# Kernel optimization log

Hardware: AMD Instinct MI355X
Metric: run time of the kernel (lower is better)

The kernel has to match this reference:

```python
import jax, jax.numpy as jnp
import numpy as np

N, E, G, B, L = 24576, 98304, 512, 512, 1000
F_IN, H1, C1, C2, HID = 5, 2, 64, 128, 256


def setup_inputs() -> dict:
    key = jax.random.key(0)
    ks = jax.random.split(key, 20)
    rn = lambda k, s: jax.random.normal(k, s, jnp.float32) * 0.1
    return {
        "x": jax.random.normal(ks[0], (N, F_IN), jnp.float32),
        "edge_index": jax.random.randint(ks[1], (2, E), 0, N),
        "batch": jnp.sort(jax.random.randint(ks[2], (N,), 0, G)),
        "protein_seq": jax.random.randint(ks[3], (B, L), 0, 22),
        "W1": rn(ks[4], (F_IN, H1 * C1)), "att_src1": rn(ks[5], (H1, C1)), "att_dst1": rn(ks[6], (H1, C1)), "b1": jnp.zeros((H1 * C1,), jnp.float32),
        "W2": rn(ks[7], (H1 * C1, C2)), "att_src2": rn(ks[8], (1, C2)), "att_dst2": rn(ks[9], (1, C2)), "b2": jnp.zeros((C2,), jnp.float32),
        "Wd": rn(ks[10], (C2, HID)), "bd": jnp.zeros((HID,), jnp.float32),
        "Pe": rn(ks[11], (22, 64)),
        "K1": rn(ks[12], (64, 64, 3)), "bk1": jnp.zeros((64,), jnp.float32),
        "K2": rn(ks[13], (128, 64, 5)), "bk2": jnp.zeros((128,), jnp.float32),
        "Wp": rn(ks[14], (128, HID)), "bp": jnp.zeros((HID,), jnp.float32),
        "Wf1": rn(ks[15], (2 * HID, 128)), "bf1": jnp.zeros((128,), jnp.float32),
        "Wf2": rn(ks[16], (128, 64)), "bf2": jnp.zeros((64,), jnp.float32),
        "Wo": rn(ks[17], (64, 1)), "bo": jnp.zeros((1,), jnp.float32),
    }


def _gat(x, edge_index, W, att_src, att_dst, b, heads, out_ch):
    """PyG GATConv: add self-loops, per-edge LeakyReLU(0.2) scores, segment softmax over dst."""
    n = x.shape[0]
    h = (x @ W).reshape(n, heads, out_ch)
    loop = jnp.arange(n)
    src = jnp.concatenate([edge_index[0], loop])
    dst = jnp.concatenate([edge_index[1], loop])
    a_s = jnp.sum(h * att_src[None], axis=-1)  # [n, H]
    a_d = jnp.sum(h * att_dst[None], axis=-1)
    e = jax.nn.leaky_relu(a_s[src] + a_d[dst], negative_slope=0.2)  # [E+n, H]
    m = jax.ops.segment_max(e, dst, num_segments=n)
    w = jnp.exp(e - m[dst])
    den = jax.ops.segment_sum(w, dst, num_segments=n)
    alpha = w / (den[dst] + 1e-16)
    out = jax.ops.segment_sum(h[src] * alpha[..., None], dst, num_segments=n)
    return out.reshape(n, heads * out_ch) + b


def _conv1d(x, k, pad):  # x: [B,C,L], k: [O,I,K]
    return jax.lax.conv_general_dilated(x, k, (1,), [(pad, pad)], dimension_numbers=("NCH", "OIH", "NCH"))


def reference(x, edge_index, batch, protein_seq, W1, att_src1, att_dst1, b1, W2, att_src2, att_dst2, b2, Wd, bd, Pe, K1, bk1, K2, bk2, Wp, bp, Wf1, bf1, Wf2, bf2, Wo, bo):
    # drug branch (GAT x2 + global mean pool)
    g = jax.nn.elu(_gat(x, edge_index, W1, att_src1, att_dst1, b1, H1, C1))
    g = jax.nn.elu(_gat(g, edge_index, W2, att_src2, att_dst2, b2, 1, C2))
    sums = jax.ops.segment_sum(g, batch, num_segments=G)
    cnt = jax.ops.segment_sum(jnp.ones((g.shape[0], 1), g.dtype), batch, num_segments=G)
    drug = jax.nn.relu(sums / jnp.maximum(cnt, 1.0) @ Wd + bd)
    # protein branch (embed -> conv1d x2 -> global max pool)
    pe = Pe[protein_seq].transpose(0, 2, 1)  # [B, 64, L]
    p = jax.nn.elu(_conv1d(pe, K1, 1) + bk1[None, :, None])
    p = jax.nn.elu(_conv1d(p, K2, 2) + bk2[None, :, None])
    prot = jax.nn.relu(jnp.max(p, axis=2) @ Wp + bp)
    # head
    h = jnp.concatenate([drug, prot], axis=1)
    h = jax.nn.relu(h @ Wf1 + bf1)
    h = jax.nn.relu(h @ Wf2 + bf2)
    return h @ Wo + bo
```

## Files before the change

### kernel.cpp

```cpp
#include <hip/hip_runtime.h>
#include <hip/hip_bf16.h>
#include <math.h>

#define NN 24576
#define NE 98304
#define ETOT (NE + NN)
#define NG 512
#define NB 512
#define LL 1000
#define TL 124
#define NTILE 9
#define PROT_BLKS (NB * NTILE)
#define CNT_BLKS (ETOT / 256)
#define AS1_BLKS (NN * 2 / 256)

typedef __attribute__((ext_vector_type(8))) short short8;
typedef __attribute__((ext_vector_type(4))) short short4v;
typedef __attribute__((ext_vector_type(4))) float f32x4;

__device__ inline short f2bf(float x) {
    union { __hip_bfloat16 b; short s; } u;
    u.b = __float2bfloat16(x);
    return u.s;
}

__device__ inline float bf2f(short s) {
    return __uint_as_float(((unsigned)(unsigned short)s) << 16);
}

__device__ inline void atomicMaxFloat(float* addr, float val) {
    int* ai = (int*)addr;
    int old = __float_as_int(*addr);
    while (__int_as_float(old) < val) {
        int assumed = old;
        old = atomicCAS(ai, assumed, __float_as_int(val));
        if (old == assumed) break;
    }
}

__global__ void k_init_prep(int* deg, int* cursor, float* sums, float* cnt, float* pmax,
                            const float* K1, const float* K2, const float* W2, const float* Pe,
                            const float* W1, const float* as1c, const float* ad1c,
                            const float* as2c, const float* ad2c,
                            short* Bswz1, short* Bswz2, short* Bh2, short* Bl2, short* Peb,
                            float* wvec) {
    int bid = blockIdx.x, t = threadIdx.x;
    if (bid < 256) {
        int i = bid * 256 + t;
        if (i < NN) { deg[i] = 0; cursor[i] = 0; }
        if (i < NG * 128) sums[i] = 0.f;
        if (i < NG) cnt[i] = 0.f;
        if (i < NB * 128) pmax[i] = -1e30f;
        return;
    }
    int idx = (bid - 256) * 256 + t;
    if (idx < 22 * 64) Peb[idx] = f2bf(Pe[idx]);
    if (idx < 20) {
        int q = idx % 10, hd = q / 5, f = q % 5;
        const float* av = (idx < 10) ? as1c : ad1c;
        float s = 0.f;
        for (int c = 0; c < 64; c++) s += W1[f * 128 + hd * 64 + c] * av[hd * 64 + c];
        wvec[idx < 10 ? q : 10 + q] = s;
    }
    if (idx >= 32 && idx < 288) {
        int q = idx - 32;
        int kk = q & 127;
        const float* av = (q < 128) ? as2c : ad2c;
        float s = 0.f;
        for (int n2 = 0; n2 < 128; n2++) s += W2[kk * 128 + n2] * av[n2];
        wvec[idx] = s;
    }
    if (idx < 192 * 64) {
        int j = idx & 7, lane = (idx >> 3) & 63, rest = idx >> 9;
        int nt = rest & 3, kb = rest >> 2;
        int k = kb * 32 + ((lane >> 4) << 3) + j;
        int n = nt * 16 + (lane & 15);
        int kk = k >> 6, i = k & 63;
        Bswz1[idx] = f2bf(K1[n * 192 + i * 3 + kk]);
    }
    if (idx < 320 * 128) {
        int j = idx & 7, lane = (idx >> 3) & 63, rest = idx >> 9;
        int nt = rest & 7, kb = rest >> 3;
        int k = kb * 32 + ((lane >> 4) << 3) + j;
        int n = nt * 16 + (lane & 15);
        int kk = k / 64, i = k % 64;
        Bswz2[idx] = f2bf(K2[n * 320 + i * 5 + kk]);
    }
    if (idx < 128 * 128) {
        int j = idx & 7, lane = (idx >> 3) & 63, rest = idx >> 9;
        int nt = rest & 7, kb = rest >> 3;
        int k = kb * 32 + ((lane >> 4) << 3) + j;
        int n = nt * 16 + (lane & 15);
        float v = W2[k * 128 + n];
        short hh = f2bf(v);
        Bh2[idx] = hh;
        Bl2[idx] = f2bf(v - bf2f(hh));
    }
}

#define SSTR 72
__global__ __launch_bounds__(256, 4) void k_prot_cnt_as1(
    const int* seq, const short* Peb, const short* Bswz1, const float* bk1,
    const short* Bswz2, const float* bk2, float* pmax,
    const int* ei, int* deg,
    const float* x, const float* wvec, float* as1o, float* ad1o) {
    int bid = blockIdx.x;
    int t = threadIdx.x;

    if (bid >= PROT_BLKS) {
        int rb = bid - PROT_BLKS;
        if (rb < CNT_BLKS) {
            int e = rb * 256 + t;
            int d = (e < NE) ? ei[NE + e] : e - NE;
            atomicAdd(&deg[d], 1);
        } else {
            int idx = (rb - CNT_BLKS) * 256 + t;
            int n = idx >> 1, hd = idx & 1;
            float s = 0.f, dv = 0.f;
#pragma unroll
            for (int f = 0; f < 5; f++) {
                float xv = x[n * 5 + f];
                s += xv * wvec[hd * 5 + f];
                dv += xv * wvec[10 + hd * 5 + f];
            }
            as1o[idx] = s;
            ad1o[idx] = dv;
        }
        return;
    }

    __shared__ __align__(16) short sEmb[130 * SSTR];
    __shared__ __align__(16) short s1[132 * SSTR];

    int b = bid / NTILE;
    int tile = bid - b * NTILE;
    int t0 = tile * TL;
    int wv = t >> 6, lane = t & 63;
    int ln15 = lane & 15, quad = lane >> 4;
    int mhalf = wv & 1, nhalf = wv >> 1;

    for (int j0 = 0; j0 < 130; j0 += 64) {
        int j = j0 + (t >> 2);
        if (j < 130) {
            int c0 = (t & 3) * 16;
            int l = t0 - 3 + j;
            int id = (l >= 0 && l < LL) ? seq[b * LL + l] : -1;
            short* dst = &sEmb[j * SSTR + c0];
            if (id >= 0) {
                const short8* src = (const short8*)&Peb[id * 64 + c0];
                *(short8*)dst = src[0];
                *(short8*)(dst + 8) = src[1];
            } else {
                *(short8*)dst = (short8){0, 0, 0, 0, 0, 0, 0, 0};
                *(short8*)(dst + 8) = (short8){0, 0, 0, 0, 0, 0, 0, 0};
            }
        }
    }
    s1[(128 + (t >> 6)) * SSTR + (t & 63)] = 0;
    __syncthreads();

    {
        f32x4 acc[4][2];
#pragma unroll
        for (int mi = 0; mi < 4; mi++)
#pragma unroll
            for (int ni = 0; ni < 2; ni++) acc[mi][ni] = (f32x4){0.f, 0.f, 0.f, 0.f};
#pragma unroll
        for (int kb = 0; kb < 6; kb++) {
            int koff = kb * 32 + quad * 8;
            int kk = koff >> 6, i0 = koff & 63;
            short8 b0 = *(const short8*)&Bswz1[((kb * 4 + nhalf * 2 + 0) * 64 + lane) * 8];
            short8 b1 = *(const short8*)&Bswz1[((kb * 4 + nhalf * 2 + 1) * 64 + lane) * 8];
#pragma unroll
            for (int mi = 0; mi < 4; mi++) {
                int arow = (mhalf * 4 + mi) * 16 + ln15 + kk;
                short8 a = *(const short8*)&sEmb[arow * SSTR + i0];
                acc[mi][0] = __builtin_amdgcn_mfma_f32_16x16x32_bf16(a, b0, acc[mi][0], 0, 0, 0);
                acc[mi][1] = __builtin_amdgcn_mfma_f32_16x16x32_bf16(a, b1, acc[mi][1], 0, 0, 0);
            }
        }
#pragma unroll
        for (int mi = 0; mi < 4; mi++) {
            int mt = mhalf * 4 + mi;
#pragma unroll
            for (int ni = 0; ni < 2; ni++) {
                int col = (nhalf * 2 + ni) * 16 + ln15;
                float bias = bk1[col];
#pragma unroll
                for (int r = 0; r < 4; r++) {
                    int q = mt * 16 + quad * 4 + r;
                    int l = t0 - 2 + q;
                    float v = acc[mi][ni][r] + bias;
                    v = v > 0.f ? v : __expf(v) - 1.f;
                    s1[q * SSTR + col] = (l >= 0 && l < LL) ? f2bf(v) : (short)0;
                }
            }
        }
    }
    __syncthreads();

    f32x4 acc2[4][4];
#pragma unroll
    for (int mi = 0; mi < 4; mi++)
#pragma unroll
        for (int ni = 0; ni < 4; ni++) acc2[mi][ni] = (f32x4){0.f, 0.f, 0.f, 0.f};
#pragma unroll 2
    for (int kb = 0; kb < 10; kb++) {
        int koff = kb * 32 + quad * 8;
        int kk = koff >> 6, i0 = koff & 63;
        short8 a[4], bb[4];
#pragma unroll
        for (int mi = 0; mi < 4; mi++) {
            int arow = (mhalf * 4 + mi) * 16 + ln15 + kk;
            a[mi] = *(const short8*)&s1[arow * SSTR + i0];
        }
#pragma unroll
        for (int ni = 0; ni < 4; ni++)
            bb[ni] = *(const short8*)&Bswz2[((kb * 8 + nhalf * 4 + ni) * 64 + lane) * 8];
#pragma unroll
        for (int mi = 0; mi < 4; mi++)
#pragma unroll
            for (int ni = 0; ni < 4; ni++)
                acc2[mi][ni] = __builtin_amdgcn_mfma_f32_16x16x32_bf16(a[mi], bb[ni], acc2[mi][ni], 0, 0, 0);
    }

#pragma unroll
    for (int ni = 0; ni < 4; ni++) {
        int col = (nhalf * 4 + ni) * 16 + ln15;
        float mx = -1e30f;
#pragma unroll
        for (int mi = 0; mi < 4; mi++) {
#pragma unroll
            for (int r = 0; r < 4; r++) {
                int p = (mhalf * 4 + mi) * 16 + quad * 4 + r;
                if (p < TL && t0 + p < LL) mx = fmaxf(mx, acc2[mi][ni][r]);
            }
        }
        mx = fmaxf(mx, __shfl_xor(mx, 16, 64));
        mx = fmaxf(mx, __shfl_xor(mx, 32, 64));
        if (quad == 0) {
            float v = mx + bk2[col];
            v = v > 0.f ? v : __expf(v) - 1.f;
            atomicMaxFloat(&pmax[b * 128 + col], v);
        }
    }
}

__global__ void k_scan1(const int* deg, int* excl, int* part) {
    __shared__ int s[256];
    int b = blockIdx.x, t = threadIdx.x, i = b * 256 + t;
    int v = deg[i];
    s[t] = v;
    __syncthreads();
    for (int o = 1; o < 256; o <<= 1) {
        int x = (t >= o) ? s[t - o] : 0;
        __syncthreads();
        s[t] += x;
        __syncthreads();
    }
    excl[i] = s[t] - v;
    if (t == 255) part[b] = s[t];
}

__global__ void k_scan23(const int* excl, const int* part, int* rowptr) {
    __shared__ int sp[96];
    __shared__ int pref;
    int b = blockIdx.x, t = threadIdx.x;
    if (t < 96) sp[t] = part[t];
    __syncthreads();
    if (t == 0) {
        int run = 0;
        for (int i = 0; i < b; i++) run += sp[i];
        pref = run;
    }
    __syncthreads();
    int i = b * 256 + t;
    rowptr[i] = excl[i] + pref;
    if (i == 0) rowptr[NN] = ETOT;
}

__global__ void k_scatter(const int* ei, const int* rowptr, int* cursor, int* colidx) {
    int e = blockIdx.x * 256 + threadIdx.x;
    if (e >= ETOT) return;
    int s, d;
    if (e < NE) { s = ei[e]; d = ei[NE + e]; }
    else { s = d = e - NE; }
    int pos = atomicAdd(&cursor[d], 1);
    colidx[rowptr[d] + pos] = s;
}

__global__ void k_agg2x(const int* rowptr, const int* colidx, const float* x,
                        const float* as_, const float* ad_,
                        const float* W1, const float* b1, const float* wvec,
                        unsigned int* g1b, float* as2, float* ad2) {
    __shared__ float sW[640];
    __shared__ float sb1[128];
    __shared__ float swa[256];
    int t = threadIdx.x;
    for (int i = t; i < 640; i += 256) sW[i] = W1[i];
    if (t < 128) { sb1[t] = b1[t]; swa[t] = wvec[32 + t]; swa[128 + t] = wvec[160 + t]; }
    __syncthreads();

    int d = blockIdx.x * 16 + (t >> 4);
    int g = t & 15;
    int hd = (g < 5) ? 0 : 1;
    int f = (g < 5) ? g : g - 5;
    float adv = ad_[d * 2 + hd];
    int p0 = rowptr[d], p1 = rowptr[d + 1];
    float den = 0.f, acc = 0.f;
    if (g < 10) {
        for (int pc = p0; pc < p1; pc += 4) {
            int sarr[4]; float ev[4], xv[4];
#pragma unroll
            for (int i = 0; i < 4; i++) {
                int pp = pc + i;
                sarr[i] = colidx[pp < p1 ? pp : p1 - 1];
            }
#pragma unroll
            for (int i = 0; i < 4; i++) {
                ev[i] = as_[sarr[i] * 2 + hd];
                xv[i] = x[sarr[i] * 5 + f];
            }
#pragma unroll
            for (int i = 0; i < 4; i++) {
                if (pc + i < p1) {
                    float e = ev[i] + adv;
                    e = e >= 0.f ? e : 0.2f * e;
                    float w = __expf(e);
                    den += w;
                    acc += w * xv[i];
                }
            }
        }
    }
    float xn = acc / (den + 1e-16f);
    int gb = (t & 63) & ~15;
    int hcol = g >> 3;
    float xs[5];
#pragma unroll
    for (int f2 = 0; f2 < 5; f2++)
        xs[f2] = __shfl(xn, gb + hcol * 5 + f2, 64);
    float ps = 0.f, pd = 0.f;
    float g1v[8];
#pragma unroll
    for (int k = 0; k < 8; k++) {
        int col = g * 8 + k;
        float v = sb1[col];
#pragma unroll
        for (int f2 = 0; f2 < 5; f2++) v += xs[f2] * sW[f2 * 128 + col];
        v = v > 0.f ? v : __expf(v) - 1.f;
        g1v[k] = v;
        ps += v * swa[col];
        pd += v * swa[128 + col];
    }
    uint4 pk;
    pk.x = ((unsigned)(unsigned short)f2bf(g1v[1]) << 16) | (unsigned)(unsigned short)f2bf(g1v[0]);
    pk.y = ((unsigned)(unsigned short)f2bf(g1v[3]) << 16) | (unsigned)(unsigned short)f2bf(g1v[2]);
    pk.z = ((unsigned)(unsigned short)f2bf(g1v[5]) << 16) | (unsigned)(unsigned short)f2bf(g1v[4]);
    pk.w = ((unsigned)(unsigned short)f2bf(g1v[7]) << 16) | (unsigned)(unsigned short)f2bf(g1v[6]);
    *(uint4*)&g1b[d * 64 + g * 4] = pk;
#pragma unroll
    for (int msk = 1; msk < 16; msk <<= 1) {
        ps += __shfl_xor(ps, msk, 64);
        pd += __shfl_xor(pd, msk, 64);
    }
    if (g == 0) { as2[d] = ps; ad2[d] = pd; }
}

__global__ void k_agg1y(const int* rowptr, const int* colidx, const unsigned int* hb,
                        const float* as_, const float* ad_, float* yacc) {
    int t = threadIdx.x;
    int d = blockIdx.x * 4 + (t >> 6);
    int c = t & 63;
    float adv = ad_[d];
    int p0 = rowptr[d], p1 = rowptr[d + 1];
    float den = 0.f, acc0 = 0.f, acc1 = 0.f;
    for (int pc = p0; pc < p1; pc += 4) {
        int sarr[4]; float ev[4]; unsigned int hv[4];
#pragma unroll
        for (int i = 0; i < 4; i++) {
            int pp = pc + i;
            sarr[i] = colidx[pp < p1 ? pp : p1 - 1];
        }
#pragma unroll
        for (int i = 0; i < 4; i++) {
            ev[i] = as_[sarr[i]];
            hv[i] = hb[sarr[i] * 64 + c];
        }
#pragma unroll
        for (int i = 0; i < 4; i++) {
            if (pc + i < p1) {
                float e = ev[i] + adv;
                e = e >= 0.f ? e : 0.2f * e;
                float w = __expf(e);
                den += w;
                acc0 += w * __uint_as_float(hv[i] << 16);
                acc1 += w * __uint_as_float(hv[i] & 0xFFFF0000u);
            }
        }
    }
    float inv = 1.f / (den + 1e-16f);
    ((float2*)yacc)[d * 64 + c] = (float2){acc0 * inv, acc1 * inv};
}

#define ASTR 136
__global__ __launch_bounds__(256, 2) void k_g2mm(
    const float* yacc, const short* Bh, const short* Bl, const float* b2, float* g2) {
    __shared__ __align__(16) short Ah[64 * ASTR];
    __shared__ __align__(16) short Al[64 * ASTR];
    int t = threadIdx.x;
    int m0 = blockIdx.x * 64;
    int wv = t >> 6, lane = t & 63;
    int ln15 = lane & 15, quad = lane >> 4;

    for (int i = t; i < 64 * 32; i += 256) {
        int row = i >> 5, c4 = (i & 31) * 4;
        float4 v = *(const float4*)&yacc[(m0 + row) * 128 + c4];
        short4v hi, lo;
        hi.x = f2bf(v.x); lo.x = f2bf(v.x - bf2f(hi.x));
        hi.y = f2bf(v.y); lo.y = f2bf(v.y - bf2f(hi.y));
        hi.z = f2bf(v.z); lo.z = f2bf(v.z - bf2f(hi.z));
        hi.w = f2bf(v.w); lo.w = f2bf(v.w - bf2f(hi.w));
        *(short4v*)&Ah[row * ASTR + c4] = hi;
        *(short4v*)&Al[row * ASTR + c4] = lo;
    }
    __syncthreads();

    f32x4 acc[8];
#pragma unroll
    for (int nt = 0; nt < 8; nt++) acc[nt] = (f32x4){0.f, 0.f, 0.f, 0.f};
    int arow = wv * 16 + ln15;
#pragma unroll
    for (int kb = 0; kb < 4; kb++) {
        int koff = kb * 32 + quad * 8;
        short8 a_hi = *(const short8*)&Ah[arow * ASTR + koff];
        short8 a_lo = *(const short8*)&Al[arow * ASTR + koff];
#pragma unroll
        for (int nt = 0; nt < 8; nt++) {
            short8 bh = *(const short8*)&Bh[((kb * 8 + nt) * 64 + lane) * 8];
            short8 bl = *(const short8*)&Bl[((kb * 8 + nt) * 64 + lane) * 8];
            acc[nt] = __builtin_amdgcn_mfma_f32_16x16x32_bf16(a_hi, bh, acc[nt], 0, 0, 0);
            acc[nt] = __builtin_amdgcn_mfma_f32_16x16x32_bf16(a_hi, bl, acc[nt], 0, 0, 0);
            acc[nt] = __builtin_amdgcn_mfma_f32_16x16x32_bf16(a_lo, bh, acc[nt], 0, 0, 0);
        }
    }
#pragma unroll
    for (int nt = 0; nt < 8; nt++) {
        int col = nt * 16 + ln15;
        float bias = b2[col];
#pragma unroll
        for (int r = 0; r < 4; r++) {
            float v = acc[nt][r] + bias;
            v = v > 0.f ? v : __expf(v) - 1.f;
            int n = m0 + wv * 16 + quad * 4 + r;
            g2[n * 128 + col] = v;
        }
    }
}

__global__ void k_pool(const float* g2, const int* batch, float* sums, float* cnt) {
    __shared__ int sb[96];
    int blk = blockIdx.x, j = threadIdx.x;
    int n0 = blk * 96;
    if (j < 96) sb[j] = batch[n0 + j];
    __syncthreads();
    float v[4];
#pragma unroll
    for (int i = 0; i < 4; i++) v[i] = g2[(n0 + i) * 128 + j];
    int cur = sb[0], runStart = 0;
    float acc = 0.f;
    for (int q0 = 0; q0 < 96; q0 += 4) {
        float nv[4] = {0.f, 0.f, 0.f, 0.f};
        if (q0 + 4 < 96) {
#pragma unroll
            for (int i = 0; i < 4; i++) nv[i] = g2[(n0 + q0 + 4 + i) * 128 + j];
        }
#pragma unroll
        for (int i = 0; i < 4; i++) {
            int q = q0 + i;
            int bb = sb[q];
            if (bb != cur) {
                atomicAdd(&sums[cur * 128 + j], acc);
                if (j == 0) atomicAdd(&cnt[cur], (float)(q - runStart));
                cur = bb; acc = 0.f; runStart = q;
            }
            acc += v[i];
        }
#pragma unroll
        for (int i = 0; i < 4; i++) v[i] = nv[i];
    }
    atomicAdd(&sums[cur * 128 + j], acc);
    if (j == 0) atomicAdd(&cnt[cur], (float)(96 - runStart));
}

__global__ __launch_bounds__(512) void k_tail(
    const float* pmax, const float* Wp, const float* bp,
    const float* sums, const float* cnt, const float* Wd, const float* bd,
    const float* Wf1, const float* bf1, const float* Wf2, const float* bf2,
    const float* Wo, const float* bo, float* out) {
    __shared__ float in2[512];
    __shared__ float part1[512];
    __shared__ float hh[128];
    __shared__ float part2[512];
    __shared__ float h2s[64];
    int g = blockIdx.x, t = threadIdx.x;

    if (t < 256) {
        float pacc = bp[t];
#pragma unroll 8
        for (int i = 0; i < 128; i++) pacc += pmax[g * 128 + i] * Wp[i * 256 + t];
        in2[256 + t] = pacc > 0.f ? pacc : 0.f;
    } else {
        int o = t - 256;
        float c = cnt[g]; c = c < 1.f ? 1.f : c;
        float inv = 1.f / c;
        float dacc = bd[o];
#pragma unroll 8
        for (int i = 0; i < 128; i++) dacc += sums[g * 128 + i] * inv * Wd[i * 256 + o];
        in2[o] = dacc > 0.f ? dacc : 0.f;
    }
    __syncthreads();

    {
        int o = t >> 2, ks = t & 3;
        float p = 0.f;
        int c0 = ks * 128;
#pragma unroll 8
        for (int cc = c0; cc < c0 + 128; cc++) p += in2[cc] * Wf1[cc * 128 + o];
        part1[t] = p;
    }
    __syncthreads();
    if (t < 128) {
        float a = bf1[t] + part1[t * 4] + part1[t * 4 + 1] + part1[t * 4 + 2] + part1[t * 4 + 3];
        hh[t] = a > 0.f ? a : 0.f;
    }
    __syncthreads();

    {
        int o = t >> 3, ks = t & 7;
        float p = 0.f;
        int c0 = ks * 16;
#pragma unroll
        for (int cc = c0; cc < c0 + 16; cc++) p += hh[cc] * Wf2[cc * 64 + o];
        part2[t] = p;
    }
    __syncthreads();
    if (t < 64) {
        float a = bf2[t];
#pragma unroll
        for (int k = 0; k < 8; k++) a += part2[t * 8 + k];
        h2s[t] = a > 0.f ? a : 0.f;
    }
    __syncthreads();

    if (t < 64) {
        float p = h2s[t] * Wo[t];
#pragma unroll
        for (int off = 32; off > 0; off >>= 1) p += __shfl_down(p, off, 64);
        if (t == 0) out[g] = p + bo[0];
    }
}

extern "C" void kernel_launch(void* const* d_in, const int* in_sizes, int n_in,
                              void* d_out, int out_size, void* d_ws, size_t ws_size,
                              hipStream_t stream) {
    (void)in_sizes; (void)n_in; (void)out_size; (void)ws_size;
    const float* x   = (const float*)d_in[0];
    const int* ei    = (const int*)d_in[1];
    const int* batch = (const int*)d_in[2];
    const int* seq   = (const int*)d_in[3];
    const float* W1  = (const float*)d_in[4];
    const float* a_s1 = (const float*)d_in[5];
    const float* a_d1 = (const float*)d_in[6];
    const float* b1  = (const float*)d_in[7];
    const float* W2  = (const float*)d_in[8];
    const float* a_s2 = (const float*)d_in[9];
    const float* a_d2 = (const float*)d_in[10];
    const float* b2  = (const float*)d_in[11];
    const float* Wd  = (const float*)d_in[12];
    const float* bd  = (const float*)d_in[13];
    const float* Pe  = (const float*)d_in[14];
    const float* K1  = (const float*)d_in[15];
    const float* bk1 = (const float*)d_in[16];
    const float* K2  = (const float*)d_in[17];
    const float* bk2 = (const float*)d_in[18];
    const float* Wp  = (const float*)d_in[19];
    const float* bp  = (const float*)d_in[20];
    const float* Wf1 = (const float*)d_in[21];
    const float* bf1 = (const float*)d_in[22];
    const float* Wf2 = (const float*)d_in[23];
    const float* bf2 = (const float*)d_in[24];
    const float* Wo  = (const float*)d_in[25];
    const float* bo  = (const float*)d_in[26];
    float* out = (float*)d_out;

    float* w = (float*)d_ws;
    float* g1bf = w; w += NN * 64;
    float* yacc = w; w += NN * 128;
    float* g2   = w; w += NN * 128;
    float* as1  = w; w += NN * 2;
    float* ad1  = w; w += NN * 2;
    float* as2  = w; w += NN;
    float* ad2  = w; w += NN;
    float* sums = w; w += NG * 128;
    float* cnt  = w; w += NG;
    float* pmax = w; w += NB * 128;
    float* wvec = w; w += 512;
    short* Bswz1 = (short*)w; w += 192 * 64 / 2;
    short* Bswz2 = (short*)w; w += 320 * 128 / 2;
    short* Bh2  = (short*)w; w += 128 * 128 / 2;
    short* Bl2  = (short*)w; w += 128 * 128 / 2;
    short* Peb  = (short*)w; w += 22 * 64 / 2 + 8;
    int* deg    = (int*)w; w += NN;
    int* cursor = (int*)w; w += NN;
    int* excl   = (int*)w; w += NN;
    int* part   = (int*)w; w += 128;
    int* rowptr = (int*)w; w += NN + 8;
    int* colidx = (int*)w; w += ETOT;

    unsigned int* g1b = (unsigned int*)g1bf;

    hipLaunchKernelGGL(k_init_prep, dim3(256 + 160), dim3(256), 0, stream,
                       deg, cursor, sums, cnt, pmax,
                       K1, K2, W2, Pe, W1, a_s1, a_d1, a_s2, a_d2,
                       Bswz1, Bswz2, Bh2, Bl2, Peb, wvec);

    hipLaunchKernelGGL(k_prot_cnt_as1, dim3(PROT_BLKS + CNT_BLKS + AS1_BLKS), dim3(256), 0, stream,
                       seq, Peb, Bswz1, bk1, Bswz2, bk2, pmax,
                       ei, deg, x, wvec, as1, ad1);

    hipLaunchKernelGGL(k_scan1, dim3(NN / 256), dim3(256), 0, stream, deg, excl, part);
    hipLaunchKernelGGL(k_scan23, dim3(NN / 256), dim3(256), 0, stream, excl, part, rowptr);
    hipLaunchKernelGGL(k_scatter, dim3(ETOT / 256), dim3(256), 0, stream, ei, rowptr, cursor, colidx);

    hipLaunchKernelGGL(k_agg2x, dim3(NN / 16), dim3(256), 0, stream,
                       rowptr, colidx, x, as1, ad1, W1, b1, wvec, g1b, as2, ad2);

    hipLaunchKernelGGL(k_agg1y, dim3(NN / 4), dim3(256), 0, stream,
                       rowptr, colidx, g1b, as2, ad2, yacc);

    hipLaunchKernelGGL(k_g2mm, dim3(NN / 64), dim3(256), 0, stream,
                       yacc, Bh2, Bl2, b2, g2);

    hipLaunchKernelGGL(k_pool, dim3(NN / 96), dim3(128), 0, stream, g2, batch, sums, cnt);

    hipLaunchKernelGGL(k_tail, dim3(NG), dim3(512), 0, stream,
                       pmax, Wp, bp, sums, cnt, Wd, bd, Wf1, bf1, Wf2, bf2, Wo, bo, out);
}
```

Before: 300.6 us.

## Fold embedding into conv1 via per-token lookup table and shrink protein tiles

Since the embedding vocabulary has only 22 tokens, conv1 of the embedded sequence is precomputed as a table M1[token][tap][out_ch] holding K1·Pe. The protein kernel then builds each conv1 output row by summing three table rows plus the bias, which replaces the MFMA conv1 stage and the staging of embeddings in shared memory. Tiles shrink from 124 to 60 positions with all four waves splitting the conv2 output channels, and the occupancy hint rises to 6 blocks. The costs are more blocks with more halo overlap (68 rows computed per 60 outputs) and a fp32 table gather in place of bf16 math, which slightly changes rounding.

After: 294.9 us. No clear change (-1.9%).

```diff
diff --git a/kernel.cpp b/kernel.cpp
--- a/kernel.cpp
+++ b/kernel.cpp
@@ -8,8 +8,8 @@
 #define NG 512
 #define NB 512
 #define LL 1000
-#define TL 124
-#define NTILE 9
+#define TL 60
+#define NTILE 17
 #define PROT_BLKS (NB * NTILE)
 #define CNT_BLKS (ETOT / 256)
 #define AS1_BLKS (NN * 2 / 256)
@@ -42,7 +42,7 @@
                             const float* K1, const float* K2, const float* W2, const float* Pe,
                             const float* W1, const float* as1c, const float* ad1c,
                             const float* as2c, const float* ad2c,
-                            short* Bswz1, short* Bswz2, short* Bh2, short* Bl2, short* Peb,
+                            short* Bswz2, short* Bh2, short* Bl2, float* M1,
                             float* wvec) {
     int bid = blockIdx.x, t = threadIdx.x;
     if (bid < 256) {
@@ -54,7 +54,6 @@
         return;
     }
     int idx = (bid - 256) * 256 + t;
-    if (idx < 22 * 64) Peb[idx] = f2bf(Pe[idx]);
     if (idx < 20) {
         int q = idx % 10, hd = q / 5, f = q % 5;
         const float* av = (idx < 10) ? as1c : ad1c;
@@ -70,13 +69,12 @@
         for (int n2 = 0; n2 < 128; n2++) s += W2[kk * 128 + n2] * av[n2];
         wvec[idx] = s;
     }
-    if (idx < 192 * 64) {
-        int j = idx & 7, lane = (idx >> 3) & 63, rest = idx >> 9;
-        int nt = rest & 3, kb = rest >> 2;
-        int k = kb * 32 + ((lane >> 4) << 3) + j;
-        int n = nt * 16 + (lane & 15);
-        int kk = k >> 6, i = k & 63;
-        Bswz1[idx] = f2bf(K1[n * 192 + i * 3 + kk]);
+    if (idx < 22 * 3 * 64) {
+        int tok = idx / 192, r2 = idx % 192;
+        int k = r2 >> 6, oc = r2 & 63;
+        float s = 0.f;
+        for (int ic = 0; ic < 64; ic++) s += K1[oc * 192 + ic * 3 + k] * Pe[tok * 64 + ic];
+        M1[idx] = s;
     }
     if (idx < 320 * 128) {
         int j = idx & 7, lane = (idx >> 3) & 63, rest = idx >> 9;
@@ -99,8 +97,8 @@
 }
 
 #define SSTR 72
-__global__ __launch_bounds__(256, 4) void k_prot_cnt_as1(
-    const int* seq, const short* Peb, const short* Bswz1, const float* bk1,
+__global__ __launch_bounds__(256, 6) void k_prot_cnt_as1(
+    const int* seq, const float* M1, const float* bk1,
     const short* Bswz2, const float* bk2, float* pmax,
     const int* ei, int* deg,
     const float* x, const float* wvec, float* as1o, float* ad1o) {
@@ -129,110 +127,96 @@
         return;
     }
 
-    __shared__ __align__(16) short sEmb[130 * SSTR];
-    __shared__ __align__(16) short s1[132 * SSTR];
+    __shared__ __align__(16) short s1[68 * SSTR];
+    __shared__ int stok[68];
 
     int b = bid / NTILE;
     int tile = bid - b * NTILE;
     int t0 = tile * TL;
+
+    if (t < 66) {
+        int l = t0 - 3 + t;
+        stok[t] = (l >= 0 && l < LL) ? seq[b * LL + l] : -1;
+    }
+    if (t < 36) {
+        *(short8*)&s1[64 * SSTR + t * 8] = (short8){0, 0, 0, 0, 0, 0, 0, 0};
+    }
+    __syncthreads();
+
+    {
+        int q = t >> 2, c0 = (t & 3) << 4;
+        int l = t0 - 2 + q;
+        short tmp[16];
+        if (l >= 0 && l < LL) {
+            float v[16];
+#pragma unroll
+            for (int j = 0; j < 4; j++) {
+                float4 bv = *(const float4*)&bk1[c0 + j * 4];
+                v[j * 4 + 0] = bv.x; v[j * 4 + 1] = bv.y; v[j * 4 + 2] = bv.z; v[j * 4 + 3] = bv.w;
+            }
+#pragma unroll
+            for (int k = 0; k < 3; k++) {
+                int tok = stok[q + k];
+                if (tok >= 0) {
+                    const float4* mr = (const float4*)&M1[tok * 192 + k * 64 + c0];
+#pragma unroll
+                    for (int j = 0; j < 4; j++) {
+                        float4 mv = mr[j];
+                        v[j * 4 + 0] += mv.x; v[j * 4 + 1] += mv.y;
+                        v[j * 4 + 2] += mv.z; v[j * 4 + 3] += mv.w;
+                    }
+                }
+            }
+#pragma unroll
+            for (int j = 0; j < 16; j++) {
+                float xv = v[j];
+                xv = xv > 0.f ? xv : __expf(xv) - 1.f;
+                tmp[j] = f2bf(xv);
+            }
+        } else {
+#pragma unroll
+            for (int j = 0; j < 16; j++) tmp[j] = 0;
+        }
+        *(short8*)&s1[q * SSTR + c0] = *(short8*)&tmp[0];
+        *(short8*)&s1[q * SSTR + c0 + 8] = *(short8*)&tmp[8];
+    }
+    __syncthreads();
+
     int wv = t >> 6, lane = t & 63;
     int ln15 = lane & 15, quad = lane >> 4;
-    int mhalf = wv & 1, nhalf = wv >> 1;
-
-    for (int j0 = 0; j0 < 130; j0 += 64) {
-        int j = j0 + (t >> 2);
-        if (j < 130) {
-            int c0 = (t & 3) * 16;
-            int l = t0 - 3 + j;
-            int id = (l >= 0 && l < LL) ? seq[b * LL + l] : -1;
-            short* dst = &sEmb[j * SSTR + c0];
-            if (id >= 0) {
-                const short8* src = (const short8*)&Peb[id * 64 + c0];
-                *(short8*)dst = src[0];
-                *(short8*)(dst + 8) = src[1];
-            } else {
-                *(short8*)dst = (short8){0, 0, 0, 0, 0, 0, 0, 0};
-                *(short8*)(dst + 8) = (short8){0, 0, 0, 0, 0, 0, 0, 0};
-            }
-        }
-    }
-    s1[(128 + (t >> 6)) * SSTR + (t & 63)] = 0;
-    __syncthreads();
-
-    {
-        f32x4 acc[4][2];
-#pragma unroll
-        for (int mi = 0; mi < 4; mi++)
-#pragma unroll
-            for (int ni = 0; ni < 2; ni++) acc[mi][ni] = (f32x4){0.f, 0.f, 0.f, 0.f};
-#pragma unroll
-        for (int kb = 0; kb < 6; kb++) {
-            int koff = kb * 32 + quad * 8;
-            int kk = koff >> 6, i0 = koff & 63;
-            short8 b0 = *(const short8*)&Bswz1[((kb * 4 + nhalf * 2 + 0) * 64 + lane) * 8];
-            short8 b1 = *(const short8*)&Bswz1[((kb * 4 + nhalf * 2 + 1) * 64 + lane) * 8];
-#pragma unroll
-            for (int mi = 0; mi < 4; mi++) {
-                int arow = (mhalf * 4 + mi) * 16 + ln15 + kk;
-                short8 a = *(const short8*)&sEmb[arow * SSTR + i0];
-                acc[mi][0] = __builtin_amdgcn_mfma_f32_16x16x32_bf16(a, b0, acc[mi][0], 0, 0, 0);
-                acc[mi][1] = __builtin_amdgcn_mfma_f32_16x16x32_bf16(a, b1, acc[mi][1], 0, 0, 0);
-            }
-        }
-#pragma unroll
-        for (int mi = 0; mi < 4; mi++) {
-            int mt = mhalf * 4 + mi;
-#pragma unroll
-            for (int ni = 0; ni < 2; ni++) {
-                int col = (nhalf * 2 + ni) * 16 + ln15;
-                float bias = bk1[col];
-#pragma unroll
-                for (int r = 0; r < 4; r++) {
-                    int q = mt * 16 + quad * 4 + r;
-                    int l = t0 - 2 + q;
-                    float v = acc[mi][ni][r] + bias;
-                    v = v > 0.f ? v : __expf(v) - 1.f;
-                    s1[q * SSTR + col] = (l >= 0 && l < LL) ? f2bf(v) : (short)0;
-                }
-            }
-        }
-    }
-    __syncthreads();
-
-    f32x4 acc2[4][4];
+
+    f32x4 acc2[4][2];
 #pragma unroll
     for (int mi = 0; mi < 4; mi++)
 #pragma unroll
-        for (int ni = 0; ni < 4; ni++) acc2[mi][ni] = (f32x4){0.f, 0.f, 0.f, 0.f};
+        for (int ni = 0; ni < 2; ni++) acc2[mi][ni] = (f32x4){0.f, 0.f, 0.f, 0.f};
 #pragma unroll 2
     for (int kb = 0; kb < 10; kb++) {
         int koff = kb * 32 + quad * 8;
         int kk = koff >> 6, i0 = koff & 63;
-        short8 a[4], bb[4];
+        short8 a[4], bb[2];
+#pragma unroll
+        for (int mi = 0; mi < 4; mi++)
+            a[mi] = *(const short8*)&s1[(mi * 16 + ln15 + kk) * SSTR + i0];
+#pragma unroll
+        for (int ni = 0; ni < 2; ni++)
+            bb[ni] = *(const short8*)&Bswz2[((kb * 8 + wv * 2 + ni) * 64 + lane) * 8];
+#pragma unroll
+        for (int mi = 0; mi < 4; mi++)
+#pragma unroll
+            for (int ni = 0; ni < 2; ni++)
+                acc2[mi][ni] = __builtin_amdgcn_mfma_f32_16x16x32_bf16(a[mi], bb[ni], acc2[mi][ni], 0, 0, 0);
+    }
+
+#pragma unroll
+    for (int ni = 0; ni < 2; ni++) {
+        int col = (wv * 2 + ni) * 16 + ln15;
+        float mx = -1e30f;
 #pragma unroll
         for (int mi = 0; mi < 4; mi++) {
-            int arow = (mhalf * 4 + mi) * 16 + ln15 + kk;
-            a[mi] = *(const short8*)&s1[arow * SSTR + i0];
-        }
-#pragma unroll
-        for (int ni = 0; ni < 4; ni++)
-            bb[ni] = *(const short8*)&Bswz2[((kb * 8 + nhalf * 4 + ni) * 64 + lane) * 8];
-#pragma unroll
-        for (int mi = 0; mi < 4; mi++)
-#pragma unroll
-            for (int ni = 0; ni < 4; ni++)
-                acc2[mi][ni] = __builtin_amdgcn_mfma_f32_16x16x32_bf16(a[mi], bb[ni], acc2[mi][ni], 0, 0, 0);
-    }
-
-#pragma unroll
-    for (int ni = 0; ni < 4; ni++) {
-        int col = (nhalf * 4 + ni) * 16 + ln15;
-        float mx = -1e30f;
-#pragma unroll
-        for (int mi = 0; mi < 4; mi++) {
 #pragma unroll
             for (int r = 0; r < 4; r++) {
-                int p = (mhalf * 4 + mi) * 16 + quad * 4 + r;
+                int p = mi * 16 + quad * 4 + r;
                 if (p < TL && t0 + p < LL) mx = fmaxf(mx, acc2[mi][ni][r]);
             }
         }
@@ -606,11 +590,10 @@
     float* cnt  = w; w += NG;
     float* pmax = w; w += NB * 128;
     float* wvec = w; w += 512;
-    short* Bswz1 = (short*)w; w += 192 * 64 / 2;
     short* Bswz2 = (short*)w; w += 320 * 128 / 2;
     short* Bh2  = (short*)w; w += 128 * 128 / 2;
     short* Bl2  = (short*)w; w += 128 * 128 / 2;
-    short* Peb  = (short*)w; w += 22 * 64 / 2 + 8;
+    float* M1   = w; w += 22 * 3 * 64;
     int* deg    = (int*)w; w += NN;
     int* cursor = (int*)w; w += NN;
     int* excl   = (int*)w; w += NN;
@@ -623,10 +606,10 @@
     hipLaunchKernelGGL(k_init_prep, dim3(256 + 160), dim3(256), 0, stream,
                        deg, cursor, sums, cnt, pmax,
                        K1, K2, W2, Pe, W1, a_s1, a_d1, a_s2, a_d2,
-                       Bswz1, Bswz2, Bh2, Bl2, Peb, wvec);
+                       Bswz2, Bh2, Bl2, M1, wvec);
 
     hipLaunchKernelGGL(k_prot_cnt_as1, dim3(PROT_BLKS + CNT_BLKS + AS1_BLKS), dim3(256), 0, stream,
-                       seq, Peb, Bswz1, bk1, Bswz2, bk2, pmax,
+                       seq, M1, bk1, Bswz2, bk2, pmax,
                        ei, deg, x, wvec, as1, ad1);
 
     hipLaunchKernelGGL(k_scan1, dim3(NN / 256), dim3(256), 0, stream, deg, excl, part);
```
